# Kernel optimization log

Measured on AMD Instinct MI355X. Metric: run time of the kernel, lower is better.

Reference implementation:

```python
import jax, jax.numpy as jnp
import numpy as np

EPS = 1e-5
K_NN = 5

def _bn(x, g, b, m, v):
    # BatchNorm1d in eval mode (running stats)
    return (x - m) * g / jnp.sqrt(v + EPS) + b

def _transf(x, w1, b1, g1, be1, m1, v1, w2, b2, g2, be2, m2, v2):
    h = jax.nn.relu(_bn(x @ w1.T + b1, g1, be1, m1, v1))
    return jax.nn.relu(_bn(h @ w2.T + b2, g2, be2, m2, v2))

def _cdist(x, y):
    # euclidean pairwise distance [Nq, Nk]
    d2 = jnp.sum(x * x, 1)[:, None] + jnp.sum(y * y, 1)[None, :] - 2.0 * (x @ y.T)
    return jnp.sqrt(jnp.clip(d2, 0.0))

def _to_pix(f):
    # [B,C,H,W] -> [B*H*W, C]
    B, C, H, W = f.shape
    return f.transpose(1, 0, 2, 3).reshape(C, -1).T

def _to_fmap(p, shape):
    B, C, H, W = shape
    return p.T.reshape(C, B, H, W).transpose(1, 0, 2, 3)

def _attend(dq, dk, aq, ak, vals, c1w, c1b, c2w, c2b):
    # full pairwise distance + hard kNN mask + softplus/softmax attention
    d = _cdist(dq, dk)                                  # [Nq, Nk]
    kth = -jax.lax.top_k(-d, K_NN)[0][:, K_NN - 1]       # K-th smallest per row
    # Conv1d(kernel_size = feat_dim) over length-feat_dim signal == dot product + bias
    att = (aq @ c1w + c1b)[:, None] + (ak @ c2w + c2b)[None, :]
    att = jax.nn.softplus(att) + jnp.where(d > kth[:, None], -1e9, 0.0)
    att = jax.nn.softmax(att, axis=1)
    return att @ vals

def _forward(inp_cont, inp_style, peers_cont, peers_style,
             w1c, b1c, g1c, be1c, m1c, v1c, w2c, b2c, g2c, be2c, m2c, v2c,
             c1cw, c1cb, c2cw, c2cb,
             w1s, b1s, g1s, be1s, m1s, v1s, w2s, b2s, g2s, be2s, m2s, v2s,
             c1sw, c1sb, c2sw, c2sb):
    ip = _to_pix(inp_cont)      # [N, C]
    pp = _to_pix(peers_cont)    # [N, C]
    ps = _to_pix(peers_style)   # [N, 2C]
    # recompose style: distance in content space, gather peer style
    aq = _transf(ip, w1c, b1c, g1c, be1c, m1c, v1c, w2c, b2c, g2c, be2c, m2c, v2c)
    ak = _transf(pp, w1c, b1c, g1c, be1c, m1c, v1c, w2c, b2c, g2c, be2c, m2c, v2c)
    out_sty = _attend(ip, pp, aq, ak, ps, c1cw, c1cb, c2cw, c2cb)   # [N, 2C]
    # recompose content: distance in (recomposed) style space, gather peer content
    sq = _transf(out_sty, w1s, b1s, g1s, be1s, m1s, v1s, w2s, b2s, g2s, be2s, m2s, v2s)
    sk = _transf(ps, w1s, b1s, g1s, be1s, m1s, v1s, w2s, b2s, g2s, be2s, m2s, v2s)
    out_cont = _attend(out_sty, ps, sq, sk, pp, c1sw, c1sb, c2sw, c2sb)  # [N, C]
    out_cont_f = _to_fmap(out_cont, inp_cont.shape)
    out_sty_f = _to_fmap(out_sty, inp_style.shape)
    return jnp.concatenate([out_cont_f, out_sty_f], axis=1)

def setup_inputs() -> dict:
    ks = jax.random.split(jax.random.key(0), 64)
    it = iter(range(64))
    rn = lambda sh, s=0.05: jax.random.normal(ks[next(it)], sh, jnp.float32) * s
    un = lambda sh: jax.random.uniform(ks[next(it)], sh, jnp.float32, 0.5, 1.5)
    C = 256; B = 1; H = W = 64
    return dict(
        inp_cont=rn((B, C, H, W), 1.0), inp_style=rn((B, 2 * C, H, W), 1.0),
        peers_cont=rn((B, C, H, W), 1.0), peers_style=rn((B, 2 * C, H, W), 1.0),
        w1c=rn((C // 2, C)), b1c=rn((C // 2,)), g1c=un((C // 2,)), be1c=rn((C // 2,)), m1c=rn((C // 2,)), v1c=un((C // 2,)),
        w2c=rn((C // 4, C // 2)), b2c=rn((C // 4,)), g2c=un((C // 4,)), be2c=rn((C // 4,)), m2c=rn((C // 4,)), v2c=un((C // 4,)),
        c1cw=rn((C // 4,)), c1cb=rn(()), c2cw=rn((C // 4,)), c2cb=rn(()),
        w1s=rn((C, 2 * C)), b1s=rn((C,)), g1s=un((C,)), be1s=rn((C,)), m1s=rn((C,)), v1s=un((C,)),
        w2s=rn((C // 2, C)), b2s=rn((C // 2,)), g2s=un((C // 2,)), be2s=rn((C // 2,)), m2s=rn((C // 2,)), v2s=un((C // 2,)),
        c1sw=rn((C // 2,)), c1sb=rn(()), c2sw=rn((C // 2,)), c2sb=rn(()),
    )

def reference(inp_cont, inp_style, peers_cont, peers_style,
              w1c, b1c, g1c, be1c, m1c, v1c, w2c, b2c, g2c, be2c, m2c, v2c,
              c1cw, c1cb, c2cw, c2cb,
              w1s, b1s, g1s, be1s, m1s, v1s, w2s, b2s, g2s, be2s, m2s, v2s,
              c1sw, c1sb, c2sw, c2sb):
    return _forward(inp_cont, inp_style, peers_cont, peers_style,
                    w1c, b1c, g1c, be1c, m1c, v1c, w2c, b2c, g2c, be2c, m2c, v2c,
                    c1cw, c1cb, c2cw, c2cb,
                    w1s, b1s, g1s, be1s, m1s, v1s, w2s, b2s, g2s, be2s, m2s, v2s,
                    c1sw, c1sb, c2sw, c2sb)
```

## Files before the change

### kernel.cpp

```cpp
#include <hip/hip_runtime.h>
#include <math.h>

#pragma clang fp contract(off)

#define NPIX 4096
#define BIGF 3.0e38f
#define SLOTS 16


__device__ __forceinline__ void ins5v(float v, float dl[5]) {
    if (v >= dl[4]) return;
    dl[4] = v;
#pragma unroll
    for (int u = 4; u > 0; --u)
        if (dl[u] < dl[u - 1]) { float t_ = dl[u]; dl[u] = dl[u - 1]; dl[u - 1] = t_; }
}

__device__ __forceinline__ float softplus_np(float x) {
    if (x > 0.f) {
        float ef = (float)exp((double)(-x));
        return x + (float)log1p((double)ef);
    } else if (x < 0.f) {
        float ef = (float)exp((double)x);
        return (float)log1p((double)ef);
    }
    return 0.69314718055994530942f;
}


__global__ __launch_bounds__(256) void gemm_bn_relu2_kernel(
    const float* __restrict__ W,
    const float* __restrict__ Xa, const float* __restrict__ Xb,
    const float* __restrict__ b, const float* __restrict__ g,
    const float* __restrict__ be, const float* __restrict__ m,
    const float* __restrict__ v,
    float* __restrict__ Ha, float* __restrict__ Hb, int M, int K) {
    const float* X = blockIdx.z ? Xb : Xa;
    float* H = blockIdx.z ? Hb : Ha;
    __shared__ float Ws[16][68];
    __shared__ float Xs[16][68];
    int t = threadIdx.x;
    int tx = t & 15, ty = t >> 4;
    int n0 = blockIdx.x * 64, m0 = blockIdx.y * 64;
    int wm = t >> 2, wk = (t & 3) * 4;
    int xk = t >> 4, xn = (t & 15) * 4;
    float acc[4][4] = {};
    for (int k0 = 0; k0 < K; k0 += 16) {
        float4 wv = *(const float4*)&W[(size_t)(m0 + wm) * K + k0 + wk];
        Ws[wk + 0][wm] = wv.x; Ws[wk + 1][wm] = wv.y;
        Ws[wk + 2][wm] = wv.z; Ws[wk + 3][wm] = wv.w;
        *(float4*)&Xs[xk][xn] = *(const float4*)&X[(size_t)(k0 + xk) * NPIX + n0 + xn];
        __syncthreads();
#pragma unroll
        for (int kk = 0; kk < 16; ++kk) {
            float4 a4 = *(float4*)&Ws[kk][ty * 4];
            float4 b4 = *(float4*)&Xs[kk][tx * 4];
            float ar[4] = {a4.x, a4.y, a4.z, a4.w};
            float br[4] = {b4.x, b4.y, b4.z, b4.w};
#pragma unroll
            for (int i = 0; i < 4; ++i)
#pragma unroll
                for (int j = 0; j < 4; ++j)
                    acc[i][j] = fmaf(ar[i], br[j], acc[i][j]);
        }
        __syncthreads();
    }
#pragma unroll
    for (int i = 0; i < 4; ++i) {
        int mrow = m0 + ty * 4 + i;
        float bb = b[mrow];
        float mm_ = m[mrow];
        float gg = g[mrow];
        float vv = v[mrow] + 1e-5f;
        float ss = (float)sqrt((double)vv);
        float bee = be[mrow];
        float o[4];
#pragma unroll
        for (int j = 0; j < 4; ++j) {
            float t0 = acc[i][j] + bb;
            t0 = t0 - mm_;
            t0 = t0 * gg;
            t0 = (float)((double)t0 / (double)ss);
            t0 = t0 + bee;
            o[j] = fmaxf(t0, 0.f);
        }
        *(float4*)&H[(size_t)mrow * NPIX + n0 + tx * 4] = *(float4*)&o[0];
    }
}


__global__ void dotk_np2_kernel(const float* __restrict__ Ha, const float* __restrict__ Hb,
                                const float* __restrict__ cwa, const float* __restrict__ cba,
                                const float* __restrict__ cwb, const float* __restrict__ cbb,
                                float* __restrict__ outa, float* __restrict__ outb, int C) {
    const float* H = blockIdx.z ? Hb : Ha;
    const float* cw = blockIdx.z ? cwb : cwa;
    const float* cb = blockIdx.z ? cbb : cba;
    float* out = blockIdx.z ? outb : outa;
    int p = blockIdx.x * 256 + threadIdx.x;
    float s = 0.f;
#pragma unroll 8
    for (int c = 0; c < C; ++c) s = fmaf(H[(size_t)c * NPIX + p], cw[c], s);
    out[p] = s + cb[0];
}


__global__ void skn_np2_kernel(const float* __restrict__ Ya, const float* __restrict__ Yb,
                               float* __restrict__ skna, float* __restrict__ sknb, int C) {
    const float* Y = blockIdx.z ? Yb : Ya;
    float* skn = blockIdx.z ? sknb : skna;
    int nb = C >> 7;
    int ppb = 256 / nb;
    int t = threadIdx.x;
    int pl = t % ppb;
    int b = t / ppb;
    int p = blockIdx.x * ppb + pl;
    __shared__ float sh[256];

    int c0 = b << 7;
    float r[8];
#pragma unroll
    for (int k = 0; k < 8; ++k) {
        float y = Y[(size_t)(c0 + k) * NPIX + p];
        r[k] = y * y;
    }
    for (int i = 8; i < 128; i += 8) {
#pragma unroll
        for (int k = 0; k < 8; ++k) {
            float y = Y[(size_t)(c0 + i + k) * NPIX + p];
            float q = y * y;
            r[k] = r[k] + q;
        }
    }
    sh[b * ppb + pl] = ((r[0] + r[1]) + (r[2] + r[3])) + ((r[4] + r[5]) + (r[6] + r[7]));
    __syncthreads();
    if (b == 0) {
        float s;
        if (nb == 2) s = sh[pl] + sh[ppb + pl];
        else s = (sh[pl] + sh[ppb + pl]) + (sh[2 * ppb + pl] + sh[3 * ppb + pl]);
        skn[p] = s;
    }
}


__global__ __launch_bounds__(256) void dist_np_kernel(
    const float* __restrict__ XT, const float* __restrict__ YT,
    const float* __restrict__ sknq, const float* __restrict__ sknk,
    float* __restrict__ D, int C, int qbase) {
    __shared__ float Xs[16][16][12];
    __shared__ float Ys[16][16][12];
    int t = threadIdx.x;
    int tx = t & 15, ty = t >> 4;
    int q0 = qbase + blockIdx.y * 128;
    int k0 = blockIdx.x * 128;
    float acc[8][8] = {};
    float4 xa = *(const float4*)&XT[(size_t)ty * NPIX + q0 + tx * 8];
    float4 xb = *(const float4*)&XT[(size_t)ty * NPIX + q0 + tx * 8 + 4];
    float4 ya = *(const float4*)&YT[(size_t)ty * NPIX + k0 + tx * 8];
    float4 yb = *(const float4*)&YT[(size_t)ty * NPIX + k0 + tx * 8 + 4];
    for (int c0 = 0; c0 < C; c0 += 16) {
        *(float4*)&Xs[ty][tx][0] = xa;
        *(float4*)&Xs[ty][tx][4] = xb;
        *(float4*)&Ys[ty][tx][0] = ya;
        *(float4*)&Ys[ty][tx][4] = yb;
        __syncthreads();
        if (c0 + 16 < C) {
            xa = *(const float4*)&XT[(size_t)(c0 + 16 + ty) * NPIX + q0 + tx * 8];
            xb = *(const float4*)&XT[(size_t)(c0 + 16 + ty) * NPIX + q0 + tx * 8 + 4];
            ya = *(const float4*)&YT[(size_t)(c0 + 16 + ty) * NPIX + k0 + tx * 8];
            yb = *(const float4*)&YT[(size_t)(c0 + 16 + ty) * NPIX + k0 + tx * 8 + 4];
        }
#pragma unroll
        for (int kk = 0; kk < 16; ++kk) {
            float4 a40 = *(float4*)&Xs[kk][ty][0];
            float4 a41 = *(float4*)&Xs[kk][ty][4];
            float4 b40 = *(float4*)&Ys[kk][tx][0];
            float4 b41 = *(float4*)&Ys[kk][tx][4];
            float ar[8] = {a40.x, a40.y, a40.z, a40.w, a41.x, a41.y, a41.z, a41.w};
            float br[8] = {b40.x, b40.y, b40.z, b40.w, b41.x, b41.y, b41.z, b41.w};
#pragma unroll
            for (int i = 0; i < 8; ++i)
#pragma unroll
                for (int j = 0; j < 8; ++j)
                    acc[i][j] = fmaf(ar[i], br[j], acc[i][j]);
        }
        __syncthreads();
    }
    float sk8[8];
    *(float4*)&sk8[0] = *(const float4*)&sknk[k0 + tx * 8];
    *(float4*)&sk8[4] = *(const float4*)&sknk[k0 + tx * 8 + 4];
#pragma unroll
    for (int i = 0; i < 8; ++i) {
        float sq = sknq[q0 + ty * 8 + i];
        int lq = q0 - qbase + ty * 8 + i;
        float tmp[8];
#pragma unroll
        for (int j = 0; j < 8; ++j) {
            float A = sq + sk8[j];
            float B = 2.0f * acc[i][j];
            float d2 = A - B;
            float dc = fmaxf(d2, 0.f);
            tmp[j] = (float)sqrt((double)dc);
        }
        *(float4*)&D[(size_t)lq * NPIX + k0 + tx * 8] = *(float4*)&tmp[0];
        *(float4*)&D[(size_t)lq * NPIX + k0 + tx * 8 + 4] = *(float4*)&tmp[4];
    }
}


__global__ __launch_bounds__(256) void row_select_np_kernel(
    const float* __restrict__ D, const float* __restrict__ qs, const float* __restrict__ ks,
    int* __restrict__ isel, float* __restrict__ wsel, int qbase) {
    int p = qbase + blockIdx.x;
    const float* drow = D + (size_t)blockIdx.x * NPIX;
    int t = threadIdx.x;
    __shared__ float tops[256][5];
    __shared__ float l2[64][5];
    __shared__ float l3[16][5];
    __shared__ float kth_sh;
    __shared__ int cnt;
    __shared__ int slotj[SLOTS];
    __shared__ int n_sh;
    __shared__ float as_[SLOTS];
    __shared__ float evs[SLOTS];
    __shared__ float mx_sh, ssum_sh;

    if (t == 0) cnt = 0;
    float vcache[16];
    *(float4*)&vcache[0] = *(const float4*)&drow[t * 16];
    *(float4*)&vcache[4] = *(const float4*)&drow[t * 16 + 4];
    *(float4*)&vcache[8] = *(const float4*)&drow[t * 16 + 8];
    *(float4*)&vcache[12] = *(const float4*)&drow[t * 16 + 12];
    float dl[5] = {BIGF, BIGF, BIGF, BIGF, BIGF};
#pragma unroll
    for (int u = 0; u < 16; ++u) ins5v(vcache[u], dl);
#pragma unroll
    for (int u = 0; u < 5; ++u) tops[t][u] = dl[u];
    __syncthreads();
    if (t < 64) {
        float md[5] = {BIGF, BIGF, BIGF, BIGF, BIGF};
        for (int i = 0; i < 4; ++i)
            for (int u = 0; u < 5; ++u) ins5v(tops[t * 4 + i][u], md);
#pragma unroll
        for (int u = 0; u < 5; ++u) l2[t][u] = md[u];
    }
    __syncthreads();
    if (t < 16) {
        float md[5] = {BIGF, BIGF, BIGF, BIGF, BIGF};
        for (int i = 0; i < 4; ++i)
            for (int u = 0; u < 5; ++u) ins5v(l2[t * 4 + i][u], md);
#pragma unroll
        for (int u = 0; u < 5; ++u) l3[t][u] = md[u];
    }
    __syncthreads();
    if (t == 0) {
        float md[5] = {BIGF, BIGF, BIGF, BIGF, BIGF};
        for (int i = 0; i < 16; ++i)
            for (int u = 0; u < 5; ++u) ins5v(l3[i][u], md);
        kth_sh = md[4];
    }
    __syncthreads();
    float kth = kth_sh;
#pragma unroll
    for (int u = 0; u < 16; ++u) {
        if (vcache[u] <= kth) {
            int s = atomicAdd(&cnt, 1);
            if (s < SLOTS) slotj[s] = t * 16 + u;
        }
    }
    __syncthreads();
    if (t == 0) {
        int n = cnt < SLOTS ? cnt : SLOTS;
        for (int a = 1; a < n; ++a) {
            int key = slotj[a]; int b = a - 1;
            while (b >= 0 && slotj[b] > key) { slotj[b + 1] = slotj[b]; --b; }
            slotj[b + 1] = key;
        }
        n_sh = n;
    }
    __syncthreads();
    int n = n_sh;
    if (t < n) {
        float x = qs[p] + ks[slotj[t]];
        as_[t] = softplus_np(x);
    }
    __syncthreads();
    if (t == 0) {
        float mx = -BIGF;
        for (int s = 0; s < n; ++s) mx = fmaxf(mx, as_[s]);
        mx_sh = mx;
    }
    __syncthreads();
    if (t < n) evs[t] = (float)exp((double)(as_[t] - mx_sh));
    __syncthreads();
    if (t == 0) {
        float bs[32];
        for (int i = 0; i < 32; ++i) bs[i] = 0.f;
        int s2 = 0;
        while (s2 < n) {
            int b = slotj[s2] >> 7;
            float r[8] = {0.f, 0.f, 0.f, 0.f, 0.f, 0.f, 0.f, 0.f};
            while (s2 < n && (slotj[s2] >> 7) == b) {
                int res = slotj[s2] & 7;
                r[res] = r[res] + evs[s2];
                ++s2;
            }
            bs[b] = ((r[0] + r[1]) + (r[2] + r[3])) + ((r[4] + r[5]) + (r[6] + r[7]));
        }
        float t16[16], t8[8], t4[4], t2[2];
        for (int i = 0; i < 16; ++i) t16[i] = bs[2 * i] + bs[2 * i + 1];
        for (int i = 0; i < 8; ++i) t8[i] = t16[2 * i] + t16[2 * i + 1];
        for (int i = 0; i < 4; ++i) t4[i] = t8[2 * i] + t8[2 * i + 1];
        for (int i = 0; i < 2; ++i) t2[i] = t4[2 * i] + t4[2 * i + 1];
        ssum_sh = t2[0] + t2[1];
    }
    __syncthreads();
    if (t < SLOTS) {
        float w = (t < n) ? (float)((double)evs[t] / (double)ssum_sh) : 0.f;
        wsel[t * NPIX + p] = w;
        isel[t * NPIX + p] = (t < n) ? slotj[t] : 0;
    }
}


__global__ void gather_np_kernel(const float* __restrict__ V,
                                 const int* __restrict__ isel, const float* __restrict__ wsel,
                                 float* __restrict__ out, int CV) {
    int g = blockIdx.x * 256 + threadIdx.x;
    int p = g & (NPIX - 1);
    int c = g >> 12;
    if (c >= CV) return;
    const float* Vc = V + (size_t)c * NPIX;
    float s = 0.f;
#pragma unroll
    for (int tt = 0; tt < SLOTS; ++tt) {
        float w = wsel[tt * NPIX + p];
        int j = isel[tt * NPIX + p];
        s = fmaf(w, Vc[j], s);
    }
    out[(size_t)c * NPIX + p] = s;
}


extern "C" void kernel_launch(void* const* d_in, const int* in_sizes, int n_in,
                              void* d_out, int out_size, void* d_ws, size_t ws_size,
                              hipStream_t stream) {
    const float* ip = (const float*)d_in[0];
    const float* pp = (const float*)d_in[2];
    const float* ps = (const float*)d_in[3];
    const float* w1c = (const float*)d_in[4];
    const float* b1c = (const float*)d_in[5];
    const float* g1c = (const float*)d_in[6];
    const float* be1c = (const float*)d_in[7];
    const float* m1c = (const float*)d_in[8];
    const float* v1c = (const float*)d_in[9];
    const float* w2c = (const float*)d_in[10];
    const float* b2c = (const float*)d_in[11];
    const float* g2c = (const float*)d_in[12];
    const float* be2c = (const float*)d_in[13];
    const float* m2c = (const float*)d_in[14];
    const float* v2c = (const float*)d_in[15];
    const float* c1cw = (const float*)d_in[16];
    const float* c1cb = (const float*)d_in[17];
    const float* c2cw = (const float*)d_in[18];
    const float* c2cb = (const float*)d_in[19];
    const float* w1s = (const float*)d_in[20];
    const float* b1s = (const float*)d_in[21];
    const float* g1s = (const float*)d_in[22];
    const float* be1s = (const float*)d_in[23];
    const float* m1s = (const float*)d_in[24];
    const float* v1s = (const float*)d_in[25];
    const float* w2s = (const float*)d_in[26];
    const float* b2s = (const float*)d_in[27];
    const float* g2s = (const float*)d_in[28];
    const float* be2s = (const float*)d_in[29];
    const float* m2s = (const float*)d_in[30];
    const float* v2s = (const float*)d_in[31];
    const float* c1sw = (const float*)d_in[32];
    const float* c1sb = (const float*)d_in[33];
    const float* c2sw = (const float*)d_in[34];
    const float* c2sb = (const float*)d_in[35];

    float* out_cont = (float*)d_out;
    float* out_sty = (float*)d_out + 256 * NPIX;

    float* ws = (float*)d_ws;
    float* QS   = ws + 0;
    float* KS   = ws + 4096;
    float* SKNQ = ws + 8192;
    float* SKNK = ws + 12288;
    float* WSEL = ws + 16384;
    int*   ISEL = (int*)(ws + 81920);
    float* H1A  = ws + 147456;
    float* H1B  = ws + 1196032;
    float* H2A  = ws + 2244608;
    float* H2B  = ws + 2768896;
    float* D    = ws + 3293184;

    size_t base = 3293184;
    int chunk = 256;
    if (ws_size >= (base + (size_t)4096 * NPIX) * 4) chunk = 4096;
    else if (ws_size >= (base + (size_t)2048 * NPIX) * 4) chunk = 2048;
    else if (ws_size >= (base + (size_t)1024 * NPIX) * 4) chunk = 1024;
    else if (ws_size >= (base + (size_t)512 * NPIX) * 4) chunk = 512;
    int nch = NPIX / chunk;

    gemm_bn_relu2_kernel<<<dim3(64, 2, 2), 256, 0, stream>>>(
        w1c, ip, pp, b1c, g1c, be1c, m1c, v1c, H1A, H1B, 128, 256);
    gemm_bn_relu2_kernel<<<dim3(64, 1, 2), 256, 0, stream>>>(
        w2c, H1A, H1B, b2c, g2c, be2c, m2c, v2c, H2A, H2B, 64, 128);
    dotk_np2_kernel<<<dim3(16, 1, 2), 256, 0, stream>>>(
        H2A, H2B, c1cw, c1cb, c2cw, c2cb, QS, KS, 64);
    skn_np2_kernel<<<dim3(32, 1, 2), 256, 0, stream>>>(ip, pp, SKNQ, SKNK, 256);
    for (int ch = 0; ch < nch; ++ch) {
        dist_np_kernel<<<dim3(32, chunk / 128), 256, 0, stream>>>(ip, pp, SKNQ, SKNK, D, 256, ch * chunk);
        row_select_np_kernel<<<chunk, 256, 0, stream>>>(D, QS, KS, ISEL, WSEL, ch * chunk);
    }
    gather_np_kernel<<<(512 * NPIX) / 256, 256, 0, stream>>>(ps, ISEL, WSEL, out_sty, 512);

    gemm_bn_relu2_kernel<<<dim3(64, 4, 2), 256, 0, stream>>>(
        w1s, out_sty, ps, b1s, g1s, be1s, m1s, v1s, H1A, H1B, 256, 512);
    gemm_bn_relu2_kernel<<<dim3(64, 2, 2), 256, 0, stream>>>(
        w2s, H1A, H1B, b2s, g2s, be2s, m2s, v2s, H2A, H2B, 128, 256);
    dotk_np2_kernel<<<dim3(16, 1, 2), 256, 0, stream>>>(
        H2A, H2B, c1sw, c1sb, c2sw, c2sb, QS, KS, 128);
    skn_np2_kernel<<<dim3(64, 1, 2), 256, 0, stream>>>(out_sty, ps, SKNQ, SKNK, 512);
    for (int ch = 0; ch < nch; ++ch) {
        dist_np_kernel<<<dim3(32, chunk / 128), 256, 0, stream>>>(out_sty, ps, SKNQ, SKNK, D, 512, ch * chunk);
        row_select_np_kernel<<<chunk, 256, 0, stream>>>(D, QS, KS, ISEL, WSEL, ch * chunk);
    }
    gather_np_kernel<<<(256 * NPIX) / 256, 256, 0, stream>>>(pp, ISEL, WSEL, out_cont, 256);
}
```

Baseline: 538.3 us.

## Shrink distance GEMM tile to 64x128 with double-buffered shared memory

Measured after the change: 561.9 us. +4.4%, slower.

```diff
diff --git a/kernel.cpp b/kernel.cpp
--- a/kernel.cpp
+++ b/kernel.cpp
@@ -5,7 +5,7 @@
 
 #define NPIX 4096
 #define BIGF 3.0e38f
-#define SLOTS 16
+#define SLOTS 8
 
 
 __device__ __forceinline__ void ins5v(float v, float dl[5]) {
@@ -147,42 +147,46 @@
     const float* __restrict__ XT, const float* __restrict__ YT,
     const float* __restrict__ sknq, const float* __restrict__ sknk,
     float* __restrict__ D, int C, int qbase) {
-    __shared__ float Xs[16][16][12];
-    __shared__ float Ys[16][16][12];
+    __shared__ float Xs[2][16][68];
+    __shared__ float Ys[2][16][16][12];
     int t = threadIdx.x;
     int tx = t & 15, ty = t >> 4;
-    int q0 = qbase + blockIdx.y * 128;
+    int q0 = qbase + blockIdx.y * 64;
     int k0 = blockIdx.x * 128;
-    float acc[8][8] = {};
-    float4 xa = *(const float4*)&XT[(size_t)ty * NPIX + q0 + tx * 8];
-    float4 xb = *(const float4*)&XT[(size_t)ty * NPIX + q0 + tx * 8 + 4];
-    float4 ya = *(const float4*)&YT[(size_t)ty * NPIX + k0 + tx * 8];
-    float4 yb = *(const float4*)&YT[(size_t)ty * NPIX + k0 + tx * 8 + 4];
-    for (int c0 = 0; c0 < C; c0 += 16) {
-        *(float4*)&Xs[ty][tx][0] = xa;
-        *(float4*)&Xs[ty][tx][4] = xb;
-        *(float4*)&Ys[ty][tx][0] = ya;
-        *(float4*)&Ys[ty][tx][4] = yb;
-        __syncthreads();
-        if (c0 + 16 < C) {
-            xa = *(const float4*)&XT[(size_t)(c0 + 16 + ty) * NPIX + q0 + tx * 8];
-            xb = *(const float4*)&XT[(size_t)(c0 + 16 + ty) * NPIX + q0 + tx * 8 + 4];
-            ya = *(const float4*)&YT[(size_t)(c0 + 16 + ty) * NPIX + k0 + tx * 8];
-            yb = *(const float4*)&YT[(size_t)(c0 + 16 + ty) * NPIX + k0 + tx * 8 + 4];
+    float acc[4][8] = {};
+    float4 xr = *(const float4*)&XT[(size_t)ty * NPIX + q0 + tx * 4];
+    float4 yr0 = *(const float4*)&YT[(size_t)ty * NPIX + k0 + tx * 8];
+    float4 yr1 = *(const float4*)&YT[(size_t)ty * NPIX + k0 + tx * 8 + 4];
+    *(float4*)&Xs[0][ty][tx * 4] = xr;
+    *(float4*)&Ys[0][ty][tx][0] = yr0;
+    *(float4*)&Ys[0][ty][tx][4] = yr1;
+    __syncthreads();
+    int nt = C >> 4;
+    for (int tt2 = 0; tt2 < nt; ++tt2) {
+        int cur = tt2 & 1;
+        if (tt2 + 1 < nt) {
+            int cn = (tt2 + 1) << 4;
+            xr = *(const float4*)&XT[(size_t)(cn + ty) * NPIX + q0 + tx * 4];
+            yr0 = *(const float4*)&YT[(size_t)(cn + ty) * NPIX + k0 + tx * 8];
+            yr1 = *(const float4*)&YT[(size_t)(cn + ty) * NPIX + k0 + tx * 8 + 4];
         }
 #pragma unroll
         for (int kk = 0; kk < 16; ++kk) {
-            float4 a40 = *(float4*)&Xs[kk][ty][0];
-            float4 a41 = *(float4*)&Xs[kk][ty][4];
-            float4 b40 = *(float4*)&Ys[kk][tx][0];
-            float4 b41 = *(float4*)&Ys[kk][tx][4];
-            float ar[8] = {a40.x, a40.y, a40.z, a40.w, a41.x, a41.y, a41.z, a41.w};
+            float4 a4 = *(float4*)&Xs[cur][kk][ty * 4];
+            float4 b40 = *(float4*)&Ys[cur][kk][tx][0];
+            float4 b41 = *(float4*)&Ys[cur][kk][tx][4];
+            float ar[4] = {a4.x, a4.y, a4.z, a4.w};
             float br[8] = {b40.x, b40.y, b40.z, b40.w, b41.x, b41.y, b41.z, b41.w};
 #pragma unroll
-            for (int i = 0; i < 8; ++i)
+            for (int i = 0; i < 4; ++i)
 #pragma unroll
                 for (int j = 0; j < 8; ++j)
                     acc[i][j] = fmaf(ar[i], br[j], acc[i][j]);
+        }
+        if (tt2 + 1 < nt) {
+            *(float4*)&Xs[cur ^ 1][ty][tx * 4] = xr;
+            *(float4*)&Ys[cur ^ 1][ty][tx][0] = yr0;
+            *(float4*)&Ys[cur ^ 1][ty][tx][4] = yr1;
         }
         __syncthreads();
     }
@@ -190,9 +194,9 @@
     *(float4*)&sk8[0] = *(const float4*)&sknk[k0 + tx * 8];
     *(float4*)&sk8[4] = *(const float4*)&sknk[k0 + tx * 8 + 4];
 #pragma unroll
-    for (int i = 0; i < 8; ++i) {
-        float sq = sknq[q0 + ty * 8 + i];
-        int lq = q0 - qbase + ty * 8 + i;
+    for (int i = 0; i < 4; ++i) {
+        float sq = sknq[q0 + ty * 4 + i];
+        int lq = q0 - qbase + ty * 4 + i;
         float tmp[8];
 #pragma unroll
         for (int j = 0; j < 8; ++j) {
@@ -219,10 +223,10 @@
     __shared__ float l3[16][5];
     __shared__ float kth_sh;
     __shared__ int cnt;
-    __shared__ int slotj[SLOTS];
+    __shared__ int slotj[16];
     __shared__ int n_sh;
-    __shared__ float as_[SLOTS];
-    __shared__ float evs[SLOTS];
+    __shared__ float as_[16];
+    __shared__ float evs[16];
     __shared__ float mx_sh, ssum_sh;
 
     if (t == 0) cnt = 0;
@@ -265,12 +269,12 @@
     for (int u = 0; u < 16; ++u) {
         if (vcache[u] <= kth) {
             int s = atomicAdd(&cnt, 1);
-            if (s < SLOTS) slotj[s] = t * 16 + u;
+            if (s < 16) slotj[s] = t * 16 + u;
         }
     }
     __syncthreads();
     if (t == 0) {
-        int n = cnt < SLOTS ? cnt : SLOTS;
+        int n = cnt < 16 ? cnt : 16;
         for (int a = 1; a < n; ++a) {
             int key = slotj[a]; int b = a - 1;
             while (b >= 0 && slotj[b] > key) { slotj[b + 1] = slotj[b]; --b; }
@@ -390,14 +394,14 @@
     float* SKNQ = ws + 8192;
     float* SKNK = ws + 12288;
     float* WSEL = ws + 16384;
-    int*   ISEL = (int*)(ws + 81920);
-    float* H1A  = ws + 147456;
-    float* H1B  = ws + 1196032;
-    float* H2A  = ws + 2244608;
-    float* H2B  = ws + 2768896;
-    float* D    = ws + 3293184;
-
-    size_t base = 3293184;
+    int*   ISEL = (int*)(ws + 49152);
+    float* H1A  = ws + 81920;
+    float* H1B  = ws + 1130496;
+    float* H2A  = ws + 2179072;
+    float* H2B  = ws + 2703360;
+    float* D    = ws + 3227648;
+
+    size_t base = 3227648;
     int chunk = 256;
     if (ws_size >= (base + (size_t)4096 * NPIX) * 4) chunk = 4096;
     else if (ws_size >= (base + (size_t)2048 * NPIX) * 4) chunk = 2048;
@@ -413,7 +417,7 @@
         H2A, H2B, c1cw, c1cb, c2cw, c2cb, QS, KS, 64);
     skn_np2_kernel<<<dim3(32, 1, 2), 256, 0, stream>>>(ip, pp, SKNQ, SKNK, 256);
     for (int ch = 0; ch < nch; ++ch) {
-        dist_np_kernel<<<dim3(32, chunk / 128), 256, 0, stream>>>(ip, pp, SKNQ, SKNK, D, 256, ch * chunk);
+        dist_np_kernel<<<dim3(32, chunk / 64), 256, 0, stream>>>(ip, pp, SKNQ, SKNK, D, 256, ch * chunk);
         row_select_np_kernel<<<chunk, 256, 0, stream>>>(D, QS, KS, ISEL, WSEL, ch * chunk);
     }
     gather_np_kernel<<<(512 * NPIX) / 256, 256, 0, stream>>>(ps, ISEL, WSEL, out_sty, 512);
@@ -426,7 +430,7 @@
         H2A, H2B, c1sw, c1sb, c2sw, c2sb, QS, KS, 128);
     skn_np2_kernel<<<dim3(64, 1, 2), 256, 0, stream>>>(out_sty, ps, SKNQ, SKNK, 512);
     for (int ch = 0; ch < nch; ++ch) {
-        dist_np_kernel<<<dim3(32, chunk / 128), 256, 0, stream>>>(out_sty, ps, SKNQ, SKNK, D, 512, ch * chunk);
+        dist_np_kernel<<<dim3(32, chunk / 64), 256, 0, stream>>>(out_sty, ps, SKNQ, SKNK, D, 512, ch * chunk);
         row_select_np_kernel<<<chunk, 256, 0, stream>>>(D, QS, KS, ISEL, WSEL, ch * chunk);
     }
     gather_np_kernel<<<(256 * NPIX) / 256, 256, 0, stream>>>(pp, ISEL, WSEL, out_cont, 256);
```
